# Optimization experiments

Hardware: AMD Instinct MI355X
Metric: run time of the kernel (lower is better)

## Reference

```python
import jax, jax.numpy as jnp
import numpy as np

D_MODEL = 1024
N_HEAD = 16
B, S = 4, 2048


def setup_inputs() -> dict:
    key = jax.random.key(0)
    ks = jax.random.split(key, 13)
    s = 1.0 / np.sqrt(D_MODEL)
    inp = {
        "query": jax.random.normal(ks[0], (B, S, D_MODEL), jnp.float32),
        "key_": jax.random.normal(ks[1], (B, S, D_MODEL), jnp.float32),
        "value": jax.random.normal(ks[2], (B, S, D_MODEL), jnp.float32),
        "mask": jax.random.randint(ks[3], (B, 1, S, S), 0, 2, jnp.int32),
        "Wq": jax.random.normal(ks[4], (D_MODEL, D_MODEL), jnp.float32) * s,
        "bq": jax.random.normal(ks[5], (D_MODEL,), jnp.float32) * 0.02,
        "Wk": jax.random.normal(ks[6], (D_MODEL, D_MODEL), jnp.float32) * s,
        "bk": jax.random.normal(ks[7], (D_MODEL,), jnp.float32) * 0.02,
        "Wv": jax.random.normal(ks[8], (D_MODEL, D_MODEL), jnp.float32) * s,
        "bv": jax.random.normal(ks[9], (D_MODEL,), jnp.float32) * 0.02,
        "Wo": jax.random.normal(ks[10], (D_MODEL, D_MODEL), jnp.float32) * s,
        "bo": jax.random.normal(ks[11], (D_MODEL,), jnp.float32) * 0.02,
    }
    return inp


def _split_heads(x):
    b, l, d = x.shape
    return x.reshape(b, l, N_HEAD, d // N_HEAD).transpose(0, 2, 1, 3)  # [B,H,S,Dh]


def reference(query, key_, value, mask, Wq, bq, Wk, bk, Wv, bv, Wo, bo):
    q = _split_heads(query @ Wq + bq)
    k = _split_heads(key_ @ Wk + bk)
    v = _split_heads(value @ Wv + bv)
    dh = q.shape[-1]
    score = jnp.einsum("bhqd,bhkd->bhqk", q, k) / jnp.sqrt(jnp.float32(dh))
    score = jnp.where(mask == 0, jnp.float32(-1e9), score)
    attn = jax.nn.softmax(score, axis=-1)
    out = jnp.einsum("bhqk,bhkd->bhqd", attn, v)  # [B,H,S,Dh]
    b, h, l, d = out.shape
    out = out.transpose(0, 2, 1, 3).reshape(b, l, h * d)
    return out @ Wo + bo
```

## Files before the change

### kernel.cpp

```cpp
#include <hip/hip_runtime.h>
#include <hip/hip_bf16.h>
#include <stdint.h>

#define D_MODEL 1024
#define NHEAD   16
#define DH      64
#define BATCH   4
#define SEQ     2048

typedef __bf16 bf16;
typedef __bf16 bf16x8 __attribute__((ext_vector_type(8)));
typedef __bf16 bf16x4 __attribute__((ext_vector_type(4)));
typedef float  f32x4  __attribute__((ext_vector_type(4)));

__device__ __forceinline__ void gload16(const void* g, void* l) {
    __builtin_amdgcn_global_load_lds((const __attribute__((address_space(1))) uint32_t*)g,
                                     (__attribute__((address_space(3))) uint32_t*)l, 16, 0, 0);
}

__global__ __launch_bounds__(256) void wt_kernel(const float* __restrict__ W,
                                                 bf16* __restrict__ Wt) {
    __shared__ float t[32][33];
    int x = threadIdx.x, y = threadIdx.y;
    int bi = blockIdx.x * 32;
    int bj = blockIdx.y * 32;
#pragma unroll
    for (int j = 0; j < 4; ++j)
        t[y + j * 8][x] = W[(bi + y + j * 8) * D_MODEL + bj + x];
    __syncthreads();
#pragma unroll
    for (int j = 0; j < 4; ++j)
        Wt[(long long)(bj + y + j * 8) * D_MODEL + bi + x] = (bf16)t[x][y + j * 8];
}

__global__ __launch_bounds__(256) void f2b_kernel(const float* __restrict__ in,
                                                  bf16* __restrict__ out) {
    long long i = ((long long)blockIdx.x * 256 + threadIdx.x) * 8;
    float4 a = *(const float4*)&in[i];
    float4 b = *(const float4*)&in[i + 4];
    bf16x8 o;
    o[0] = (bf16)a.x; o[1] = (bf16)a.y; o[2] = (bf16)a.z; o[3] = (bf16)a.w;
    o[4] = (bf16)b.x; o[5] = (bf16)b.y; o[6] = (bf16)b.z; o[7] = (bf16)b.w;
    *(bf16x8*)&out[i] = o;
}

__global__ __launch_bounds__(256) void maskpack_kernel(const int* __restrict__ mask,
                                                       unsigned* __restrict__ bits) {
    long long tid = (long long)blockIdx.x * 256 + threadIdx.x;
    int lane = threadIdx.x & 63;
    long long wid = tid >> 6;
    int m = mask[wid * 64 + lane];
    unsigned long long bal = __ballot(m != 0);
    if (lane == 0) *(unsigned long long*)&bits[wid * 2] = bal;
}

template <int OUT_MODE>
__global__ __launch_bounds__(256) void gemm_kernel(const bf16* __restrict__ A,
                                                   const bf16* __restrict__ Bt,
                                                   const float* __restrict__ bias,
                                                   void* __restrict__ Cptr) {
    constexpr int K = D_MODEL;
    __shared__ bf16 As[128][32];
    __shared__ bf16 Bs[128][32];
    int tid = threadIdx.x;
    int l = tid & 63, w = tid >> 6;
    int g = l >> 4, c = l & 15;
    int wm = (w >> 1) * 64, wn = (w & 1) * 64;
    long long m0 = (long long)blockIdx.y * 128;
    int n0 = blockIdx.x * 128;
    int srow = l >> 2, scolb = (l & 3) * 16;

    f32x4 acc[4][4] = {};

    for (int k0 = 0; k0 < K; k0 += 32) {
#pragma unroll
        for (int i = 0; i < 2; ++i) {
            int ck = w * 2 + i;
            int row = ck * 16 + srow;
            gload16((const char*)(A + (m0 + row) * K + k0) + scolb,
                    (char*)&As[0][0] + ck * 1024);
            gload16((const char*)(Bt + (long long)(n0 + row) * K + k0) + scolb,
                    (char*)&Bs[0][0] + ck * 1024);
        }
        __syncthreads();
        bf16x8 af[4], bfr[4];
#pragma unroll
        for (int i = 0; i < 4; ++i) af[i] = *(const bf16x8*)&As[wm + i * 16 + c][g * 8];
#pragma unroll
        for (int i = 0; i < 4; ++i) bfr[i] = *(const bf16x8*)&Bs[wn + i * 16 + c][g * 8];
#pragma unroll
        for (int mi = 0; mi < 4; ++mi)
#pragma unroll
            for (int ni = 0; ni < 4; ++ni)
                acc[mi][ni] = __builtin_amdgcn_mfma_f32_16x16x32_bf16(af[mi], bfr[ni],
                                                                     acc[mi][ni], 0, 0, 0);
        __syncthreads();
    }

#pragma unroll
    for (int mi = 0; mi < 4; ++mi) {
#pragma unroll
        for (int ni = 0; ni < 4; ++ni) {
            int n = n0 + wn + ni * 16 + c;
            float bv = bias[n];
#pragma unroll
            for (int r = 0; r < 4; ++r) {
                long long m = m0 + wm + mi * 16 + g * 4 + r;
                float val = acc[mi][ni][r] + bv;
                if constexpr (OUT_MODE == 2) {
                    ((float*)Cptr)[m * D_MODEL + n] = val;
                } else {
                    int b = (int)(m >> 11), s = (int)(m & 2047);
                    int h = n >> 6, f = n & 63;
                    long long addr;
                    if constexpr (OUT_MODE == 0)
                        addr = ((long long)(b * NHEAD + h) * SEQ + s) * DH + f;
                    else
                        addr = ((long long)(b * NHEAD + h) * DH + f) * SEQ + s;
                    ((bf16*)Cptr)[addr] = (bf16)val;
                }
            }
        }
    }
}

__global__ __launch_bounds__(256) void attn_kernel(const bf16* __restrict__ Q,
                                                   const bf16* __restrict__ Kt,
                                                   const bf16* __restrict__ Vt,
                                                   const unsigned* __restrict__ bits,
                                                   bf16* __restrict__ O) {
    __shared__ bf16 Ks[2][64][64];
    __shared__ bf16 Vs[2][64][64];
    __shared__ bf16 Ps[4][16][64];
    int tid = threadIdx.x;
    int l = tid & 63, w = tid >> 6;
    int g = l >> 4, c = l & 15;
    int bh = blockIdx.y;
    int b = bh >> 4, h = bh & 15;
    int q0 = blockIdx.x * 64;
    int q = q0 + w * 16 + c;

    const long long kbase = (long long)bh * SEQ * DH;
    const long long vbase = (long long)bh * DH * SEQ;

    bf16x8 qf0, qf1;
    {
        long long base = ((long long)bh * SEQ + q) * DH + g * 8;
        qf0 = *(const bf16x8*)&Q[base];
        qf1 = *(const bf16x8*)&Q[base + 32];
    }

    int srow = l >> 3;
    int scolb = ((l & 7) ^ srow) * 16;

    f32x4 o_acc[4] = {};
    float m_run = -INFINITY, l_run = 0.f;
    const unsigned* mrow = &bits[((long long)b * SEQ + q) * (SEQ / 32)];
    int gx8 = (g ^ (c & 7)) * 8;
    int pswz = (c & 7) * 8;

    auto stage = [&](int buf, int kv0) {
#pragma unroll
        for (int i = 0; i < 2; ++i) {
            int ck = w * 2 + i;
            int row = ck * 8 + srow;
            gload16((const char*)(Kt + kbase + (long long)(kv0 + row) * DH) + scolb,
                    (char*)&Ks[buf][0][0] + ck * 1024);
            gload16((const char*)(Vt + vbase + (long long)row * SEQ + kv0) + scolb,
                    (char*)&Vs[buf][0][0] + ck * 1024);
        }
    };
    stage(0, 0);

    int cur = 0;
    for (int t = 0; t < SEQ / 64; ++t) {
        __syncthreads();
        if (t + 1 < SEQ / 64) stage(cur ^ 1, (t + 1) * 64);

        f32x4 sacc[4] = {};
#pragma unroll
        for (int nb = 0; nb < 4; ++nb) {
            bf16x8 k0f = *(const bf16x8*)&Ks[cur][nb * 16 + c][gx8];
            bf16x8 k1f = *(const bf16x8*)&Ks[cur][nb * 16 + c][gx8 ^ 32];
            sacc[nb] = __builtin_amdgcn_mfma_f32_16x16x32_bf16(k0f, qf0, sacc[nb], 0, 0, 0);
            sacc[nb] = __builtin_amdgcn_mfma_f32_16x16x32_bf16(k1f, qf1, sacc[nb], 0, 0, 0);
        }

        uint2 mb = *(const uint2*)&mrow[t * 2];
        unsigned wsel[4] = { mb.x >> (g * 4), mb.x >> (16 + g * 4),
                             mb.y >> (g * 4), mb.y >> (16 + g * 4) };
        float pmax = -INFINITY;
#pragma unroll
        for (int nb = 0; nb < 4; ++nb)
#pragma unroll
            for (int r = 0; r < 4; ++r) {
                float s = sacc[nb][r] * 0.125f;
                s = ((wsel[nb] >> r) & 1u) ? s : -1e9f;
                sacc[nb][r] = s;
                pmax = fmaxf(pmax, s);
            }
        pmax = fmaxf(pmax, __shfl_xor(pmax, 16));
        pmax = fmaxf(pmax, __shfl_xor(pmax, 32));

        if (__any(pmax > m_run + 8.f)) {
            float mnew = fmaxf(m_run, pmax);
            float sc_own = __expf(m_run - mnew);
            m_run = mnew;
            l_run *= sc_own;
#pragma unroll
            for (int r = 0; r < 4; ++r) {
                float sc = __shfl(sc_own, g * 4 + r);
#pragma unroll
                for (int fb = 0; fb < 4; ++fb) o_acc[fb][r] *= sc;
            }
        }

        float tsum = 0.f;
#pragma unroll
        for (int nb = 0; nb < 4; ++nb) {
            bf16x4 pk;
#pragma unroll
            for (int r = 0; r < 4; ++r) {
                float p = __expf(sacc[nb][r] - m_run);
                tsum += p;
                pk[r] = (bf16)p;
            }
            *(bf16x4*)&Ps[w][c][(nb * 16 + g * 4) ^ pswz] = pk;
        }
        tsum += __shfl_xor(tsum, 16);
        tsum += __shfl_xor(tsum, 32);
        l_run += tsum;

#pragma unroll
        for (int kvb = 0; kvb < 2; ++kvb) {
            bf16x8 pf = *(const bf16x8*)&Ps[w][c][((kvb * 4 + g) ^ (c & 7)) * 8];
#pragma unroll
            for (int fb = 0; fb < 4; ++fb) {
                bf16x8 vf = *(const bf16x8*)&Vs[cur][fb * 16 + c][((kvb * 4 + g) ^ (c & 7)) * 8];
                o_acc[fb] = __builtin_amdgcn_mfma_f32_16x16x32_bf16(pf, vf, o_acc[fb], 0, 0, 0);
            }
        }
        cur ^= 1;
    }

    float linv[4];
#pragma unroll
    for (int r = 0; r < 4; ++r) linv[r] = 1.0f / __shfl(l_run, g * 4 + r);
#pragma unroll
    for (int fb = 0; fb < 4; ++fb)
#pragma unroll
        for (int r = 0; r < 4; ++r) {
            int qq = q0 + w * 16 + g * 4 + r;
            O[((long long)b * SEQ + qq) * D_MODEL + h * DH + fb * 16 + c] =
                (bf16)(o_acc[fb][r] * linv[r]);
        }
}

extern "C" void kernel_launch(void* const* d_in, const int* in_sizes, int n_in,
                              void* d_out, int out_size, void* d_ws, size_t ws_size,
                              hipStream_t stream) {
    const float* query = (const float*)d_in[0];
    const float* key_  = (const float*)d_in[1];
    const float* value = (const float*)d_in[2];
    const int*   mask  = (const int*)d_in[3];
    const float* Wq = (const float*)d_in[4];
    const float* bq = (const float*)d_in[5];
    const float* Wk = (const float*)d_in[6];
    const float* bk = (const float*)d_in[7];
    const float* Wv = (const float*)d_in[8];
    const float* bv = (const float*)d_in[9];
    const float* Wo = (const float*)d_in[10];
    const float* bo = (const float*)d_in[11];
    float* out = (float*)d_out;

    char* ws = (char*)d_ws;
    bf16* Q16  = (bf16*)(ws);
    bf16* K16  = (bf16*)(ws + (16ll << 20));
    bf16* V16t = (bf16*)(ws + (32ll << 20));
    bf16* O16  = (bf16*)(ws + (48ll << 20));
    bf16* WtQ  = (bf16*)(ws + (64ll << 20));
    bf16* WtK  = (bf16*)(ws + (66ll << 20));
    bf16* WtV  = (bf16*)(ws + (68ll << 20));
    bf16* WtO  = (bf16*)(ws + (70ll << 20));
    unsigned* bits = (unsigned*)(ws + (72ll << 20));
    bf16* Qb = (bf16*)(ws + (76ll << 20));
    bf16* Kb = (bf16*)(ws + (92ll << 20));
    bf16* Vb = (bf16*)(ws + (108ll << 20));

    dim3 tb(32, 8), tg(32, 32);
    wt_kernel<<<tg, tb, 0, stream>>>(Wq, WtQ);
    wt_kernel<<<tg, tb, 0, stream>>>(Wk, WtK);
    wt_kernel<<<tg, tb, 0, stream>>>(Wv, WtV);
    wt_kernel<<<tg, tb, 0, stream>>>(Wo, WtO);

    maskpack_kernel<<<65536, 256, 0, stream>>>(mask, bits);

    f2b_kernel<<<4096, 256, 0, stream>>>(query, Qb);
    f2b_kernel<<<4096, 256, 0, stream>>>(key_,  Kb);
    f2b_kernel<<<4096, 256, 0, stream>>>(value, Vb);

    dim3 gg(D_MODEL / 128, (BATCH * SEQ) / 128);
    gemm_kernel<0><<<gg, 256, 0, stream>>>(Qb, WtQ, bq, Q16);
    gemm_kernel<0><<<gg, 256, 0, stream>>>(Kb, WtK, bk, K16);
    gemm_kernel<1><<<gg, 256, 0, stream>>>(Vb, WtV, bv, V16t);

    attn_kernel<<<dim3(SEQ / 64, BATCH * NHEAD), 256, 0, stream>>>(Q16, K16, V16t, bits, O16);

    gemm_kernel<2><<<gg, 256, 0, stream>>>(O16, WtO, bo, out);
}
```

Measured before the change: 491.2 us.

## Batch QKV projections into one launch, enlarge attention blocks, defer masking

Merges the three fp32-to-bf16 conversions and the three QKV GEMMs into single batched launches. It folds the 1/sqrt(dh) scale into the Q projection and writes V in row layout, then transposes it with a separate LDS-tiled kernel instead of scattered strided stores. The attention kernel now uses 512-thread blocks covering 128 queries each, swizzles block order for K/V cache reuse, and applies the mask after exponentiation instead of before the max. Deferring the mask means the running max can include masked scores, which risks underflow when masked entries dominate.

New measurement: 466.3 us. 5.1% less time.

```diff
diff --git a/kernel.cpp b/kernel.cpp
--- a/kernel.cpp
+++ b/kernel.cpp
@@ -33,15 +33,20 @@
         Wt[(long long)(bj + y + j * 8) * D_MODEL + bi + x] = (bf16)t[x][y + j * 8];
 }
 
-__global__ __launch_bounds__(256) void f2b_kernel(const float* __restrict__ in,
-                                                  bf16* __restrict__ out) {
-    long long i = ((long long)blockIdx.x * 256 + threadIdx.x) * 8;
+__global__ __launch_bounds__(256) void f2b3_kernel(const float* __restrict__ q,
+                                                   const float* __restrict__ k,
+                                                   const float* __restrict__ v,
+                                                   bf16* __restrict__ out) {
+    int third = blockIdx.x >> 12;
+    int wi = blockIdx.x & 4095;
+    const float* in = third == 0 ? q : (third == 1 ? k : v);
+    long long i = (long long)wi * 2048 + threadIdx.x * 8;
     float4 a = *(const float4*)&in[i];
     float4 b = *(const float4*)&in[i + 4];
     bf16x8 o;
     o[0] = (bf16)a.x; o[1] = (bf16)a.y; o[2] = (bf16)a.z; o[3] = (bf16)a.w;
     o[4] = (bf16)b.x; o[5] = (bf16)b.y; o[6] = (bf16)b.z; o[7] = (bf16)b.w;
-    *(bf16x8*)&out[i] = o;
+    *(bf16x8*)&out[(long long)third * (8192ll * 1024) + i] = o;
 }
 
 __global__ __launch_bounds__(256) void maskpack_kernel(const int* __restrict__ mask,
@@ -54,11 +59,78 @@
     if (lane == 0) *(unsigned long long*)&bits[wid * 2] = bal;
 }
 
-template <int OUT_MODE>
-__global__ __launch_bounds__(256) void gemm_kernel(const bf16* __restrict__ A,
-                                                   const bf16* __restrict__ Bt,
-                                                   const float* __restrict__ bias,
-                                                   void* __restrict__ Cptr) {
+__global__ __launch_bounds__(256) void gemm_qkv_kernel(const bf16* __restrict__ A3,
+                                                       const bf16* __restrict__ Wt3,
+                                                       const float* __restrict__ bq,
+                                                       const float* __restrict__ bk,
+                                                       const float* __restrict__ bv,
+                                                       bf16* __restrict__ out3) {
+    constexpr int K = D_MODEL;
+    __shared__ bf16 As[128][32];
+    __shared__ bf16 Bs[128][32];
+    int tid = threadIdx.x;
+    int l = tid & 63, w = tid >> 6;
+    int g = l >> 4, c = l & 15;
+    int wm = (w >> 1) * 64, wn = (w & 1) * 64;
+    int third = blockIdx.y >> 6;
+    long long m0 = (long long)(blockIdx.y & 63) * 128;
+    int n0 = blockIdx.x * 128;
+    const bf16* A  = A3  + (long long)third * (8192ll * 1024);
+    const bf16* Bt = Wt3 + (long long)third * (1024ll * 1024);
+    const float* bias = third == 0 ? bq : (third == 1 ? bk : bv);
+    float osc = third == 0 ? 0.125f : 1.0f;
+    bf16* C = out3 + (long long)third * (8192ll * 1024);
+    int srow = l >> 2, scolb = (l & 3) * 16;
+
+    f32x4 acc[4][4] = {};
+
+    for (int k0 = 0; k0 < K; k0 += 32) {
+#pragma unroll
+        for (int i = 0; i < 2; ++i) {
+            int ck = w * 2 + i;
+            int row = ck * 16 + srow;
+            gload16((const char*)(A + (m0 + row) * K + k0) + scolb,
+                    (char*)&As[0][0] + ck * 1024);
+            gload16((const char*)(Bt + (long long)(n0 + row) * K + k0) + scolb,
+                    (char*)&Bs[0][0] + ck * 1024);
+        }
+        __syncthreads();
+        bf16x8 af[4], bfr[4];
+#pragma unroll
+        for (int i = 0; i < 4; ++i) af[i] = *(const bf16x8*)&As[wm + i * 16 + c][g * 8];
+#pragma unroll
+        for (int i = 0; i < 4; ++i) bfr[i] = *(const bf16x8*)&Bs[wn + i * 16 + c][g * 8];
+#pragma unroll
+        for (int mi = 0; mi < 4; ++mi)
+#pragma unroll
+            for (int ni = 0; ni < 4; ++ni)
+                acc[mi][ni] = __builtin_amdgcn_mfma_f32_16x16x32_bf16(af[mi], bfr[ni],
+                                                                     acc[mi][ni], 0, 0, 0);
+        __syncthreads();
+    }
+
+#pragma unroll
+    for (int mi = 0; mi < 4; ++mi) {
+#pragma unroll
+        for (int ni = 0; ni < 4; ++ni) {
+            int n = n0 + wn + ni * 16 + c;
+            float bv_ = bias[n];
+            int h = n >> 6, f = n & 63;
+#pragma unroll
+            for (int r = 0; r < 4; ++r) {
+                long long m = m0 + wm + mi * 16 + g * 4 + r;
+                float val = (acc[mi][ni][r] + bv_) * osc;
+                int b = (int)(m >> 11), s = (int)(m & 2047);
+                C[((long long)(b * NHEAD + h) * SEQ + s) * DH + f] = (bf16)val;
+            }
+        }
+    }
+}
+
+__global__ __launch_bounds__(256) void gemm_out_kernel(const bf16* __restrict__ A,
+                                                       const bf16* __restrict__ Bt,
+                                                       const float* __restrict__ bias,
+                                                       float* __restrict__ Cptr) {
     constexpr int K = D_MODEL;
     __shared__ bf16 As[128][32];
     __shared__ bf16 Bs[128][32];
@@ -98,7 +170,7 @@
     }
 
 #pragma unroll
-    for (int mi = 0; mi < 4; ++mi) {
+    for (int mi = 0; mi < 4; ++mi)
 #pragma unroll
         for (int ni = 0; ni < 4; ++ni) {
             int n = n0 + wn + ni * 16 + c;
@@ -106,38 +178,51 @@
 #pragma unroll
             for (int r = 0; r < 4; ++r) {
                 long long m = m0 + wm + mi * 16 + g * 4 + r;
-                float val = acc[mi][ni][r] + bv;
-                if constexpr (OUT_MODE == 2) {
-                    ((float*)Cptr)[m * D_MODEL + n] = val;
-                } else {
-                    int b = (int)(m >> 11), s = (int)(m & 2047);
-                    int h = n >> 6, f = n & 63;
-                    long long addr;
-                    if constexpr (OUT_MODE == 0)
-                        addr = ((long long)(b * NHEAD + h) * SEQ + s) * DH + f;
-                    else
-                        addr = ((long long)(b * NHEAD + h) * DH + f) * SEQ + s;
-                    ((bf16*)Cptr)[addr] = (bf16)val;
-                }
-            }
-        }
-    }
-}
-
-__global__ __launch_bounds__(256) void attn_kernel(const bf16* __restrict__ Q,
+                Cptr[m * D_MODEL + n] = acc[mi][ni][r] + bv;
+            }
+        }
+}
+
+__global__ __launch_bounds__(256) void vtrans_kernel(const bf16* __restrict__ in,
+                                                     bf16* __restrict__ out) {
+    __shared__ bf16 t[64][72];
+    int bh = blockIdx.y;
+    int s0 = blockIdx.x * 64;
+    int tid = threadIdx.x;
+#pragma unroll
+    for (int i = 0; i < 2; ++i) {
+        int ck = tid + i * 256;
+        int s = ck >> 3, f0 = (ck & 7) * 8;
+        bf16x8 v = *(const bf16x8*)&in[((long long)bh * SEQ + s0 + s) * DH + f0];
+#pragma unroll
+        for (int j = 0; j < 8; ++j) t[f0 + j][s] = v[j];
+    }
+    __syncthreads();
+#pragma unroll
+    for (int i = 0; i < 2; ++i) {
+        int ck = tid + i * 256;
+        int f = ck >> 3, c0 = (ck & 7) * 8;
+        bf16x8 v = *(const bf16x8*)&t[f][c0];
+        *(bf16x8*)&out[((long long)bh * DH + f) * SEQ + s0 + c0] = v;
+    }
+}
+
+__global__ __launch_bounds__(512) void attn_kernel(const bf16* __restrict__ Q,
                                                    const bf16* __restrict__ Kt,
                                                    const bf16* __restrict__ Vt,
                                                    const unsigned* __restrict__ bits,
                                                    bf16* __restrict__ O) {
     __shared__ bf16 Ks[2][64][64];
     __shared__ bf16 Vs[2][64][64];
-    __shared__ bf16 Ps[4][16][64];
+    __shared__ bf16 Ps[8][16][64];
     int tid = threadIdx.x;
     int l = tid & 63, w = tid >> 6;
     int g = l >> 4, c = l & 15;
-    int bh = blockIdx.y;
+    int orig = blockIdx.x;
+    int swz = (orig & 7) * 128 + (orig >> 3);
+    int bh = swz >> 4, qb = swz & 15;
     int b = bh >> 4, h = bh & 15;
-    int q0 = blockIdx.x * 64;
+    int q0 = qb * 128;
     int q = q0 + w * 16 + c;
 
     const long long kbase = (long long)bh * SEQ * DH;
@@ -150,25 +235,19 @@
         qf1 = *(const bf16x8*)&Q[base + 32];
     }
 
-    int srow = l >> 3;
-    int scolb = ((l & 7) ^ srow) * 16;
+    int row = tid >> 3;
+    int scolb = ((tid & 7) ^ (row & 7)) * 16;
 
     f32x4 o_acc[4] = {};
     float m_run = -INFINITY, l_run = 0.f;
     const unsigned* mrow = &bits[((long long)b * SEQ + q) * (SEQ / 32)];
     int gx8 = (g ^ (c & 7)) * 8;
-    int pswz = (c & 7) * 8;
 
     auto stage = [&](int buf, int kv0) {
-#pragma unroll
-        for (int i = 0; i < 2; ++i) {
-            int ck = w * 2 + i;
-            int row = ck * 8 + srow;
-            gload16((const char*)(Kt + kbase + (long long)(kv0 + row) * DH) + scolb,
-                    (char*)&Ks[buf][0][0] + ck * 1024);
-            gload16((const char*)(Vt + vbase + (long long)row * SEQ + kv0) + scolb,
-                    (char*)&Vs[buf][0][0] + ck * 1024);
-        }
+        gload16((const char*)(Kt + kbase + (long long)(kv0 + row) * DH) + scolb,
+                (char*)&Ks[buf][0][0] + w * 1024);
+        gload16((const char*)(Vt + vbase + (long long)row * SEQ + kv0) + scolb,
+                (char*)&Vs[buf][0][0] + w * 1024);
     };
     stage(0, 0);
 
@@ -186,19 +265,11 @@
             sacc[nb] = __builtin_amdgcn_mfma_f32_16x16x32_bf16(k1f, qf1, sacc[nb], 0, 0, 0);
         }
 
-        uint2 mb = *(const uint2*)&mrow[t * 2];
-        unsigned wsel[4] = { mb.x >> (g * 4), mb.x >> (16 + g * 4),
-                             mb.y >> (g * 4), mb.y >> (16 + g * 4) };
-        float pmax = -INFINITY;
+        float pmax = sacc[0][0];
 #pragma unroll
         for (int nb = 0; nb < 4; ++nb)
 #pragma unroll
-            for (int r = 0; r < 4; ++r) {
-                float s = sacc[nb][r] * 0.125f;
-                s = ((wsel[nb] >> r) & 1u) ? s : -1e9f;
-                sacc[nb][r] = s;
-                pmax = fmaxf(pmax, s);
-            }
+            for (int r = 0; r < 4; ++r) pmax = fmaxf(pmax, sacc[nb][r]);
         pmax = fmaxf(pmax, __shfl_xor(pmax, 16));
         pmax = fmaxf(pmax, __shfl_xor(pmax, 32));
 
@@ -215,6 +286,9 @@
             }
         }
 
+        uint2 mb = *(const uint2*)&mrow[t * 2];
+        unsigned wsel[4] = { mb.x >> (g * 4), mb.x >> (16 + g * 4),
+                             mb.y >> (g * 4), mb.y >> (16 + g * 4) };
         float tsum = 0.f;
 #pragma unroll
         for (int nb = 0; nb < 4; ++nb) {
@@ -222,10 +296,11 @@
 #pragma unroll
             for (int r = 0; r < 4; ++r) {
                 float p = __expf(sacc[nb][r] - m_run);
+                p = ((wsel[nb] >> r) & 1u) ? p : 0.f;
                 tsum += p;
                 pk[r] = (bf16)p;
             }
-            *(bf16x4*)&Ps[w][c][(nb * 16 + g * 4) ^ pswz] = pk;
+            *(bf16x4*)&Ps[w][c][(nb * 16 + g * 4) ^ ((c & 7) * 8)] = pk;
         }
         tsum += __shfl_xor(tsum, 16);
         tsum += __shfl_xor(tsum, 32);
@@ -274,37 +349,31 @@
     float* out = (float*)d_out;
 
     char* ws = (char*)d_ws;
-    bf16* Q16  = (bf16*)(ws);
-    bf16* K16  = (bf16*)(ws + (16ll << 20));
-    bf16* V16t = (bf16*)(ws + (32ll << 20));
-    bf16* O16  = (bf16*)(ws + (48ll << 20));
-    bf16* WtQ  = (bf16*)(ws + (64ll << 20));
-    bf16* WtK  = (bf16*)(ws + (66ll << 20));
-    bf16* WtV  = (bf16*)(ws + (68ll << 20));
-    bf16* WtO  = (bf16*)(ws + (70ll << 20));
-    unsigned* bits = (unsigned*)(ws + (72ll << 20));
-    bf16* Qb = (bf16*)(ws + (76ll << 20));
-    bf16* Kb = (bf16*)(ws + (92ll << 20));
-    bf16* Vb = (bf16*)(ws + (108ll << 20));
+    bf16* A3    = (bf16*)(ws);
+    bf16* V16t  = (bf16*)(ws);
+    bf16* O16   = (bf16*)(ws + (16ll << 20));
+    bf16* Q16   = (bf16*)(ws + (48ll << 20));
+    bf16* K16   = (bf16*)(ws + (64ll << 20));
+    bf16* V16   = (bf16*)(ws + (80ll << 20));
+    bf16* Wt3   = (bf16*)(ws + (96ll << 20));
+    bf16* WtO   = (bf16*)(ws + (102ll << 20));
+    unsigned* bits = (unsigned*)(ws + (104ll << 20));
 
     dim3 tb(32, 8), tg(32, 32);
-    wt_kernel<<<tg, tb, 0, stream>>>(Wq, WtQ);
-    wt_kernel<<<tg, tb, 0, stream>>>(Wk, WtK);
-    wt_kernel<<<tg, tb, 0, stream>>>(Wv, WtV);
+    wt_kernel<<<tg, tb, 0, stream>>>(Wq, Wt3);
+    wt_kernel<<<tg, tb, 0, stream>>>(Wk, Wt3 + 1024ll * 1024);
+    wt_kernel<<<tg, tb, 0, stream>>>(Wv, Wt3 + 2048ll * 1024);
     wt_kernel<<<tg, tb, 0, stream>>>(Wo, WtO);
 
     maskpack_kernel<<<65536, 256, 0, stream>>>(mask, bits);
 
-    f2b_kernel<<<4096, 256, 0, stream>>>(query, Qb);
-    f2b_kernel<<<4096, 256, 0, stream>>>(key_,  Kb);
-    f2b_kernel<<<4096, 256, 0, stream>>>(value, Vb);
-
-    dim3 gg(D_MODEL / 128, (BATCH * SEQ) / 128);
-    gemm_kernel<0><<<gg, 256, 0, stream>>>(Qb, WtQ, bq, Q16);
-    gemm_kernel<0><<<gg, 256, 0, stream>>>(Kb, WtK, bk, K16);
-    gemm_kernel<1><<<gg, 256, 0, stream>>>(Vb, WtV, bv, V16t);
-
-    attn_kernel<<<dim3(SEQ / 64, BATCH * NHEAD), 256, 0, stream>>>(Q16, K16, V16t, bits, O16);
-
-    gemm_kernel<2><<<gg, 256, 0, stream>>>(O16, WtO, bo, out);
-}
+    f2b3_kernel<<<12288, 256, 0, stream>>>(query, key_, value, A3);
+
+    gemm_qkv_kernel<<<dim3(8, 192), 256, 0, stream>>>(A3, Wt3, bq, bk, bv, Q16);
+
+    vtrans_kernel<<<dim3(32, 64), 256, 0, stream>>>(V16, V16t);
+
+    attn_kernel<<<1024, 512, 0, stream>>>(Q16, K16, V16t, bits, O16);
+
+    gemm_out_kernel<<<dim3(8, 64), 256, 0, stream>>>(O16, WtO, bo, out);
+}
```
